# Optimization experiments

Hardware: AMD Instinct MI355X
Metric: run time of the kernel (lower is better)

The kernel has to match this reference:

```python
import jax, jax.numpy as jnp
import numpy as np

BLOCK_M = 64
BLOCK_N = 64
CAUSAL = True


def setup_inputs() -> dict:
    key = jax.random.key(0)
    kq, kk, kv, km = jax.random.split(key, 4)
    B, T, H, Dqk, Dv = 2, 2048, 16, 128, 128
    q = jax.random.normal(kq, (B, T, H, Dqk), dtype=jnp.float16)
    k = jax.random.normal(kk, (B, T, H, Dqk), dtype=jnp.float16)
    v = jax.random.normal(kv, (B, T, H, Dv), dtype=jnp.float16)
    nq = T // BLOCK_M  # 32 query blocks
    nk = T // BLOCK_N  # 32 kv blocks
    block_mask = jax.random.randint(km, (B, H, nq, nk), 0, 2).astype(bool)
    # force diagonal blocks on so every (causal) query row has >=1 valid key
    eye = jnp.eye(nq, nk, dtype=bool)
    block_mask = block_mask | eye[None, None, :, :]
    return {"q": q, "k": k, "v": v, "block_mask": block_mask}


def reference(q, k, v, block_mask):
    B, T, H, Dqk = q.shape
    Dv = v.shape[-1]
    scale = 1.0 / np.sqrt(Dqk).astype(np.float32)
    qf = q.astype(jnp.float32)
    kf = k.astype(jnp.float32)
    vf = v.astype(jnp.float32)
    # groups == 1: k/v already have H heads
    scores = jnp.einsum('bthd,bshd->bhts', qf, kf) * scale  # [B,H,T,T]
    # expand block mask [B,H,nq,nk] -> [B,H,T,T]
    mask = jnp.repeat(jnp.repeat(block_mask, BLOCK_M, axis=2), BLOCK_N, axis=3)
    if CAUSAL:
        causal = jnp.tril(jnp.ones((T, T), dtype=bool))
        mask = mask & causal[None, None, :, :]
    scores = jnp.where(mask, scores, -jnp.inf)
    weights = jax.nn.softmax(scores, axis=-1)
    out = jnp.einsum('bhts,bshd->bthd', weights, vf)
    return out.astype(jnp.float16)
```

## Files before the change

### kernel.cpp

```cpp
#include <hip/hip_runtime.h>


typedef _Float16 half8 __attribute__((ext_vector_type(8)));
typedef float floatx16 __attribute__((ext_vector_type(16)));

#define B_ 2
#define T_ 2048
#define H_ 16
#define D_ 128
#define BM 64
#define BN 64
#define NQ (T_ / BM)
#define NK (T_ / BN)
#define NITEMS (B_ * H_ * NQ)
#define PSTR 40
#define TILE_HALVES 8192

#define GLOAD_LDS16(g, l) \
    __builtin_amdgcn_global_load_lds((const __attribute__((address_space(1))) void*)(g), \
                                     (__attribute__((address_space(3))) void*)(l), 16, 0, 0)

__device__ inline half8 cvt8(const float4 a, const float4 b) {
    half8 r;
    r[0] = (_Float16)a.x; r[1] = (_Float16)a.y;
    r[2] = (_Float16)a.z; r[3] = (_Float16)a.w;
    r[4] = (_Float16)b.x; r[5] = (_Float16)b.y;
    r[6] = (_Float16)b.z; r[7] = (_Float16)b.w;
    return r;
}

__device__ inline int vswz(int d) {
    return (((d & 7) ^ ((d >> 3) & 7)) << 3);
}

__global__ __launch_bounds__(256)
void cast_kv_kernel(const float* __restrict__ kg, const float* __restrict__ vg,
                    const int* __restrict__ maskg,
                    _Float16* __restrict__ wsk, _Float16* __restrict__ wsv,
                    int* __restrict__ ws_act, int* __restrict__ ws_ctr)
{
    const int tile = blockIdx.x;
    const int pair = tile >> 5;
    const int j    = tile & 31;
    const int b    = pair >> 4;
    const int h    = pair & 15;
    const int tid  = threadIdx.x;

    const size_t rowstr = H_ * D_;
    const size_t base = ((size_t)b * T_ + (size_t)j * BN) * rowstr + (size_t)h * D_;
    _Float16* imk = wsk + (size_t)tile * TILE_HALVES;
    _Float16* imv = wsv + (size_t)tile * TILE_HALVES;

    #pragma unroll
    for (int kk = 0; kk < 4; ++kk) {
        const int c  = tid + 256 * kk;
        const int s  = c >> 4;
        const int d8 = (c & 15) << 3;
        const float* kp = kg + base + (size_t)s * rowstr + d8;
        float4 a  = *(const float4*)kp;
        float4 bb = *(const float4*)(kp + 4);
        *(half8*)(&imk[s * 128 + (d8 ^ ((s & 7) << 3))]) = cvt8(a, bb);
    }
    const int vd  = (tid & 63) * 2;
    const int vsg = tid >> 6;
    #pragma unroll
    for (int p = 0; p < 2; ++p) {
        half8 r0, r1;
        #pragma unroll
        for (int i = 0; i < 8; ++i) {
            const float* vp = vg + base + (size_t)(vsg * 16 + p * 8 + i) * rowstr + vd;
            float2 vv = *(const float2*)vp;
            r0[i] = (_Float16)vv.x;
            r1[i] = (_Float16)vv.y;
        }
        const int sb = vsg * 16 + p * 8;
        *(half8*)(&imv[vd * 64 + (sb ^ vswz(vd))])           = r0;
        *(half8*)(&imv[(vd + 1) * 64 + (sb ^ vswz(vd + 1))]) = r1;
    }

    if (tid < 64) {
        int pred = 0;
        if (tid < 32 && tid <= j)
            pred = (maskg[(((size_t)b * H_ + h) * NQ + j) * NK + tid] != 0);
        unsigned long long bal = __ballot(pred);
        if (tid == 0) ws_act[(31 - j) * 32 + pair] = (int)(unsigned)bal;
    }
    if (tile == 0 && tid == 0) *ws_ctr = 0;
}

__global__ __launch_bounds__(256, 2)
void bsattn_kernel(const float* __restrict__ qg,
                   const _Float16* __restrict__ wsk,
                   const _Float16* __restrict__ wsv,
                   const int* __restrict__ ws_act,
                   int* __restrict__ ws_ctr,
                   float* __restrict__ outg)
{
    const int tid  = threadIdx.x;
    const int wave = tid >> 6;
    const int wr   = wave >> 1;
    const int wc   = wave & 1;
    const int lane = tid & 63;
    const int l31  = lane & 31;
    const int hi   = lane >> 5;

    __shared__ _Float16 smem[2 * 16384 + 4 * 32 * PSTR];
    __shared__ int sh_next;
    _Float16* Pw = smem + 2 * 16384 + wave * (32 * PSTR);

    const float cs2 = 0.08838834764831845f * 1.44269504088896341f;
    const float C2  = 6.0f * 1.44269504088896341f;

    half8 ones8;
    #pragma unroll
    for (int e = 0; e < 8; ++e) ones8[e] = (_Float16)1.0f;

    auto stage = [&](size_t tb, int j, int bet) {
        const _Float16* imk = wsk + tb + (size_t)j * TILE_HALVES;
        const _Float16* imv = wsv + tb + (size_t)j * TILE_HALVES;
        _Float16* Kb = smem + bet * 16384;
        _Float16* Vb = Kb + 8192;
        #pragma unroll
        for (int i = 0; i < 4; ++i) {
            const int off = wave * 2048 + i * 512;
            GLOAD_LDS16(imk + off + lane * 8, Kb + off);
            GLOAD_LDS16(imv + off + lane * 8, Vb + off);
        }
    };

    half8 qf[8];
    auto loadQ = [&](int bb, int hh, int qq) {
        const int qrow = qq * BM + wr * 32 + l31;
        const float* qp = qg + (((size_t)bb * T_ + qrow) * H_ + hh) * D_;
        #pragma unroll
        for (int kc = 0; kc < 8; ++kc) {
            float4 a = *(const float4*)(qp + kc * 16 + hi * 8);
            float4 c = *(const float4*)(qp + kc * 16 + hi * 8 + 4);
            qf[kc] = cvt8(a, c);
        }
    };

    if (tid == 0) sh_next = atomicAdd(ws_ctr, 1);
    __syncthreads();
    int item = sh_next;
    if (item >= NITEMS) return;

    int qi   = 31 - (item >> 5);
    int pair = item & 31;
    int b    = pair >> 4;
    int h    = pair & 15;
    size_t tilebase = (size_t)pair * NK * TILE_HALVES;
    unsigned act = (unsigned)ws_act[item];
    int jcur = __ffs(act) - 1;
    unsigned rem = act & (act - 1);
    int beta = 0;
    stage(tilebase, jcur, 0);
    loadQ(b, h, qi);

    #pragma unroll 1
    while (true) {
        bool grab_pending = (rem == 0);

        floatx16 acc[4];
        #pragma unroll
        for (int u = 0; u < 4; ++u) acc[u] = (floatx16)0.0f;
        floatx16 lacc0 = (floatx16)0.0f;
        floatx16 lacc1 = (floatx16)0.0f;

        int nit = NITEMS;
        int nqi = 0, npair = 0;
        size_t ntb = 0;
        unsigned nact = 0;

        while (true) {
            __syncthreads();

            int jnext = -1;
            if (rem) {
                jnext = __ffs(rem) - 1;
                rem &= rem - 1;
                if (rem == 0 && tid == 0) sh_next = atomicAdd(ws_ctr, 1);
                stage(tilebase, jnext, beta ^ 1);
            } else {
                if (grab_pending) {
                    if (tid == 0) sh_next = atomicAdd(ws_ctr, 1);
                    __syncthreads();
                }
                nit = sh_next;
                if (nit < NITEMS) {
                    nqi   = 31 - (nit >> 5);
                    npair = nit & 31;
                    ntb   = (size_t)npair * NK * TILE_HALVES;
                    nact  = (unsigned)ws_act[nit];
                    stage(ntb, __ffs(nact) - 1, beta ^ 1);
                }
            }

            const _Float16* Kb = smem + beta * 16384;
            const _Float16* Vb = Kb + 8192;
            const bool diag = (jcur == qi);

            if (!(diag && wc > wr)) {
                floatx16 s0 = (floatx16)0.0f, s1 = (floatx16)0.0f;
                {
                    const _Float16* Krow = Kb + (32 * wc + l31) * 128;
                    const int ksw = (l31 & 7) << 3;
                    #pragma unroll
                    for (int kc = 0; kc < 4; ++kc) {
                        half8 kf = *(const half8*)(Krow + ((kc * 16 + hi * 8) ^ ksw));
                        s0 = __builtin_amdgcn_mfma_f32_32x32x16_f16(qf[kc], kf, s0, 0, 0, 0);
                    }
                    #pragma unroll
                    for (int kc = 4; kc < 8; ++kc) {
                        half8 kf = *(const half8*)(Krow + ((kc * 16 + hi * 8) ^ ksw));
                        s1 = __builtin_amdgcn_mfma_f32_32x32x16_f16(qf[kc], kf, s1, 0, 0, 0);
                    }
                }
                floatx16 sacc = s0 + s1;

                if (diag && wc == wr) {
                    #pragma unroll
                    for (int r = 0; r < 16; ++r) {
                        const int rq = (r & 3) + 8 * (r >> 2) + 4 * hi;
                        if (l31 > rq) sacc[r] = -INFINITY;
                    }
                }

                #pragma unroll
                for (int r = 0; r < 16; ++r) {
                    const int rq = (r & 3) + 8 * (r >> 2) + 4 * hi;
                    const float p = __builtin_amdgcn_exp2f(__builtin_fmaf(sacc[r], cs2, -C2));
                    Pw[rq * PSTR + l31] = (_Float16)p;
                }

                half8 pf[2];
                #pragma unroll
                for (int kvc = 0; kvc < 2; ++kvc)
                    pf[kvc] = *(const half8*)(&Pw[l31 * PSTR + kvc * 16 + hi * 8]);

                lacc0 = __builtin_amdgcn_mfma_f32_32x32x16_f16(ones8, pf[0], lacc0, 0, 0, 0);
                lacc1 = __builtin_amdgcn_mfma_f32_32x32x16_f16(ones8, pf[1], lacc1, 0, 0, 0);

                #pragma unroll
                for (int dt = 0; dt < 4; ++dt) {
                    const int d  = dt * 32 + l31;
                    const int sw = vswz(d);
                    const _Float16* Vrow = Vb + d * 64;
                    #pragma unroll
                    for (int kvc = 0; kvc < 2; ++kvc) {
                        half8 vf = *(const half8*)(Vrow + ((32 * wc + kvc * 16 + hi * 8) ^ sw));
                        acc[dt] = __builtin_amdgcn_mfma_f32_32x32x16_f16(vf, pf[kvc], acc[dt], 0, 0, 0);
                    }
                }
            }

            if (jnext < 0) break;
            jcur = jnext;
            beta ^= 1;
        }

        if (nit < NITEMS) loadQ(npair >> 4, npair & 15, nqi);

        __syncthreads();
        float* Ebuf = (float*)(smem + beta * 16384);
        float* Lbuf = (float*)(smem + 2 * 16384);

        #pragma unroll
        for (int dt = 0; dt < 4; ++dt) {
            if ((dt >> 1) != wc) {
                const int tt = dt & 1;
                #pragma unroll
                for (int g = 0; g < 4; ++g) {
                    float4 val;
                    val.x = acc[dt][4 * g + 0];
                    val.y = acc[dt][4 * g + 1];
                    val.z = acc[dt][4 * g + 2];
                    val.w = acc[dt][4 * g + 3];
                    const int idx = (((((wr * 2 + wc) * 2 + tt) * 4 + g) * 2 + hi) * 32 + l31);
                    *(float4*)(&Ebuf[idx * 4]) = val;
                }
            }
        }
        const float lmine = lacc0[0] + lacc1[0];
        Lbuf[(wr * 2 + wc) * 32 + l31] = lmine;
        __syncthreads();

        const float ltot = lmine + Lbuf[(wr * 2 + (1 - wc)) * 32 + l31];
        const float inv  = 1.0f / ltot;
        const int qrow   = qi * BM + wr * 32 + l31;
        float* op = outg + (((size_t)b * T_ + qrow) * H_ + h) * D_;

        #pragma unroll
        for (int dt = 0; dt < 4; ++dt) {
            if ((dt >> 1) == wc) {
                const int tt = dt & 1;
                #pragma unroll
                for (int g = 0; g < 4; ++g) {
                    const int idx = (((((wr * 2 + (1 - wc)) * 2 + tt) * 4 + g) * 2 + hi) * 32 + l31);
                    float4 p = *(const float4*)(&Ebuf[idx * 4]);
                    float4 o;
                    o.x = (acc[dt][4 * g + 0] + p.x) * inv;
                    o.y = (acc[dt][4 * g + 1] + p.y) * inv;
                    o.z = (acc[dt][4 * g + 2] + p.z) * inv;
                    o.w = (acc[dt][4 * g + 3] + p.w) * inv;
                    *(float4*)(op + dt * 32 + g * 8 + hi * 4) = o;
                }
            }
        }

        if (nit >= NITEMS) return;

        item = nit;
        qi   = nqi;
        pair = npair;
        b    = pair >> 4;
        h    = pair & 15;
        tilebase = ntb;
        jcur = __ffs(nact) - 1;
        rem  = nact & (nact - 1);
        beta ^= 1;
    }
}

extern "C" void kernel_launch(void* const* d_in, const int* in_sizes, int n_in,
                              void* d_out, int out_size, void* d_ws, size_t ws_size,
                              hipStream_t stream) {
    const float* q  = (const float*)d_in[0];
    const float* k  = (const float*)d_in[1];
    const float* v  = (const float*)d_in[2];
    const int* mask = (const int*)d_in[3];
    float* out      = (float*)d_out;

    _Float16* wsk = (_Float16*)d_ws;
    _Float16* wsv = wsk + (size_t)B_ * H_ * NK * TILE_HALVES;
    int* ws_act   = (int*)(wsv + (size_t)B_ * H_ * NK * TILE_HALVES);
    int* ws_ctr   = ws_act + NITEMS;

    cast_kv_kernel<<<dim3(B_ * H_ * NK), 256, 0, stream>>>(k, v, mask, wsk, wsv,
                                                           ws_act, ws_ctr);
    bsattn_kernel<<<dim3(512), 256, 0, stream>>>(q, wsk, wsv, ws_act, ws_ctr, out);
}
```

Measured before the change: 179.7 us.

## Partition persistent work queue per XCD so each die handles four (b,h) pairs

Replaces the single global atomic work counter with eight per-XCD counters and queues, each holding four (batch, head) pairs ordered by descending query block. Workgroups choose their queue from blockIdx.x & 7, which assumes round-robin dispatch of workgroups across the eight XCDs. The aim is to keep each pair's K/V tiles resident in one XCD's L2 and to reduce atomic contention. The cost is losing global load balancing: an XCD that finishes early cannot take work from another XCD's queue.

After: 176.1 us. 1.02x faster.

```diff
diff --git a/kernel.cpp b/kernel.cpp
--- a/kernel.cpp
+++ b/kernel.cpp
@@ -12,7 +12,9 @@
 #define BN 64
 #define NQ (T_ / BM)
 #define NK (T_ / BN)
-#define NITEMS (B_ * H_ * NQ)
+#define NXCD 8
+#define PPX 4
+#define NLOCAL (PPX * NQ)
 #define PSTR 40
 #define TILE_HALVES 8192
 
@@ -83,9 +85,10 @@
         if (tid < 32 && tid <= j)
             pred = (maskg[(((size_t)b * H_ + h) * NQ + j) * NK + tid] != 0);
         unsigned long long bal = __ballot(pred);
-        if (tid == 0) ws_act[(31 - j) * 32 + pair] = (int)(unsigned)bal;
+        if (tid == 0)
+            ws_act[(pair >> 2) * NLOCAL + (31 - j) * PPX + (pair & 3)] = (int)(unsigned)bal;
     }
-    if (tile == 0 && tid == 0) *ws_ctr = 0;
+    if (tile < NXCD && tid == 0) ws_ctr[tile] = 0;
 }
 
 __global__ __launch_bounds__(256, 2)
@@ -96,6 +99,10 @@
                    int* __restrict__ ws_ctr,
                    float* __restrict__ outg)
 {
+    const int xcd  = blockIdx.x & 7;
+    int* ctr = ws_ctr + xcd;
+    const int* act_q = ws_act + xcd * NLOCAL;
+
     const int tid  = threadIdx.x;
     const int wave = tid >> 6;
     const int wr   = wave >> 1;
@@ -140,17 +147,17 @@
         }
     };
 
-    if (tid == 0) sh_next = atomicAdd(ws_ctr, 1);
+    if (tid == 0) sh_next = atomicAdd(ctr, 1);
     __syncthreads();
-    int item = sh_next;
-    if (item >= NITEMS) return;
-
-    int qi   = 31 - (item >> 5);
-    int pair = item & 31;
+    int rank = sh_next;
+    if (rank >= NLOCAL) return;
+
+    int qi   = 31 - (rank >> 2);
+    int pair = xcd * PPX + (rank & 3);
     int b    = pair >> 4;
     int h    = pair & 15;
     size_t tilebase = (size_t)pair * NK * TILE_HALVES;
-    unsigned act = (unsigned)ws_act[item];
+    unsigned act = (unsigned)act_q[rank];
     int jcur = __ffs(act) - 1;
     unsigned rem = act & (act - 1);
     int beta = 0;
@@ -167,7 +174,7 @@
         floatx16 lacc0 = (floatx16)0.0f;
         floatx16 lacc1 = (floatx16)0.0f;
 
-        int nit = NITEMS;
+        int nrank = NLOCAL;
         int nqi = 0, npair = 0;
         size_t ntb = 0;
         unsigned nact = 0;
@@ -179,19 +186,19 @@
             if (rem) {
                 jnext = __ffs(rem) - 1;
                 rem &= rem - 1;
-                if (rem == 0 && tid == 0) sh_next = atomicAdd(ws_ctr, 1);
+                if (rem == 0 && tid == 0) sh_next = atomicAdd(ctr, 1);
                 stage(tilebase, jnext, beta ^ 1);
             } else {
                 if (grab_pending) {
-                    if (tid == 0) sh_next = atomicAdd(ws_ctr, 1);
+                    if (tid == 0) sh_next = atomicAdd(ctr, 1);
                     __syncthreads();
                 }
-                nit = sh_next;
-                if (nit < NITEMS) {
-                    nqi   = 31 - (nit >> 5);
-                    npair = nit & 31;
+                nrank = sh_next;
+                if (nrank < NLOCAL) {
+                    nqi   = 31 - (nrank >> 2);
+                    npair = xcd * PPX + (nrank & 3);
                     ntb   = (size_t)npair * NK * TILE_HALVES;
-                    nact  = (unsigned)ws_act[nit];
+                    nact  = (unsigned)act_q[nrank];
                     stage(ntb, __ffs(nact) - 1, beta ^ 1);
                 }
             }
@@ -259,7 +266,7 @@
             beta ^= 1;
         }
 
-        if (nit < NITEMS) loadQ(npair >> 4, npair & 15, nqi);
+        if (nrank < NLOCAL) loadQ(npair >> 4, npair & 15, nqi);
 
         __syncthreads();
         float* Ebuf = (float*)(smem + beta * 16384);
@@ -308,9 +315,9 @@
             }
         }
 
-        if (nit >= NITEMS) return;
-
-        item = nit;
+        if (nrank >= NLOCAL) return;
+
+        rank = nrank;
         qi   = nqi;
         pair = npair;
         b    = pair >> 4;
@@ -334,7 +341,7 @@
     _Float16* wsk = (_Float16*)d_ws;
     _Float16* wsv = wsk + (size_t)B_ * H_ * NK * TILE_HALVES;
     int* ws_act   = (int*)(wsv + (size_t)B_ * H_ * NK * TILE_HALVES);
-    int* ws_ctr   = ws_act + NITEMS;
+    int* ws_ctr   = ws_act + NXCD * NLOCAL;
 
     cast_kv_kernel<<<dim3(B_ * H_ * NK), 256, 0, stream>>>(k, v, mask, wsk, wsv,
                                                            ws_act, ws_ctr);
```
